# Kernel optimization log

Hardware: AMD Instinct MI355X
Metric: run time of the kernel (lower is better)

## Reference

```python
import jax, jax.numpy as jnp
import numpy as np

VOCAB = 32000
EMB = 256
DEC = 1024
ENC = 1024  # 2 * encoder hidden (bi-directional)
B = 128
S = 512


def setup_inputs() -> dict:
    key = jax.random.key(0)
    ks = jax.random.split(key, 16)
    s = 0.02
    return {
        "inputs": jax.random.randint(ks[0], (B, 1), 0, VOCAB),
        "decoder_hidden": jax.random.normal(ks[1], (B, DEC), jnp.float32),
        "encoder_output": jax.random.normal(ks[2], (B, S, ENC), jnp.float32),
        "emb": jax.random.normal(ks[3], (VOCAB, EMB), jnp.float32) * s,
        "W1": jax.random.normal(ks[4], (ENC, DEC), jnp.float32) * s,
        "b1": jnp.zeros((DEC,), jnp.float32),
        "W2": jax.random.normal(ks[5], (DEC, DEC), jnp.float32) * s,
        "b2": jnp.zeros((DEC,), jnp.float32),
        "Wv": jax.random.normal(ks[6], (DEC, 1), jnp.float32) * s,
        "bv": jnp.zeros((1,), jnp.float32),
        "lstm_k": jax.random.normal(ks[7], (ENC + EMB, 4 * DEC), jnp.float32) * s,
        "lstm_rk": jax.random.normal(ks[8], (DEC, 4 * DEC), jnp.float32) * s,
        "lstm_b": jnp.zeros((4 * DEC,), jnp.float32),
        "fc_W": jax.random.normal(ks[9], (DEC, VOCAB), jnp.float32) * s,
        "fc_b": jnp.zeros((VOCAB,), jnp.float32),
    }


def reference(inputs, decoder_hidden, encoder_output, emb, W1, b1, W2, b2,
              Wv, bv, lstm_k, lstm_rk, lstm_b, fc_W, fc_b):
    # Bahdanau additive attention
    # score: (B, S, 1)
    hidden_proj = decoder_hidden @ W2 + b2                      # (B, DEC)
    score = jnp.tanh(encoder_output @ W1 + b1 + hidden_proj[:, None, :]) @ Wv + bv
    attention_weights = jax.nn.softmax(score, axis=1)           # (B, S, 1)
    context = jnp.sum(attention_weights * encoder_output, axis=1)  # (B, ENC)

    # embedding lookup of the single input token, concat [context, embed]
    x = jnp.concatenate([context, emb[inputs[:, 0]]], axis=-1)  # (B, ENC+EMB)

    # single-step LSTM. Original calls rnn(inputs) with NO initial_state,
    # so h0 = c0 = 0 and the recurrent kernel contributes nothing this step.
    z = x @ lstm_k + lstm_b + jnp.zeros((B, DEC), x.dtype) @ lstm_rk  # (B, 4*DEC)
    i, f, g, o = jnp.split(z, 4, axis=-1)  # keras gate order i,f,c,o
    c = jax.nn.sigmoid(f) * 0.0 + jax.nn.sigmoid(i) * jnp.tanh(g)
    h = jax.nn.sigmoid(o) * jnp.tanh(c)

    logits = h @ fc_W + fc_b                                    # (B, VOCAB)
    return logits, (h, c), attention_weights
```

## Files before the change

### kernel.cpp

```cpp
#include <hip/hip_runtime.h>
#include <hip/hip_bf16.h>
#include <stdint.h>

#define VOCAB 32000
#define EMB   256
#define DEC   1024
#define ENC   1024
#define BB    128
#define SS    512
#define MTOT  (BB * SS)
#define XCOLS (ENC + EMB)
#define NG    (4 * DEC)

typedef _Float16 half8  __attribute__((ext_vector_type(8)));
typedef _Float16 half4  __attribute__((ext_vector_type(4)));
typedef float    floatx4 __attribute__((ext_vector_type(4)));

__device__ __forceinline__ float fast_tanh(float x) {
    float e = __builtin_amdgcn_exp2f(x * 2.885390082f);
    return 1.0f - 2.0f * __builtin_amdgcn_rcpf(e + 1.0f);
}
__device__ __forceinline__ float fast_sigmoid(float x) {
    float e = __builtin_amdgcn_exp2f(-x * 1.442695041f);
    return __builtin_amdgcn_rcpf(1.0f + e);
}

__device__ __forceinline__ void gl_lds16(const void* g, void* l) {
    __builtin_amdgcn_global_load_lds(
        (const __attribute__((address_space(1))) uint32_t*)g,
        (__attribute__((address_space(3))) uint32_t*)l,
        16, 0, 0);
}

__global__ void k_transpose_w1(const float* __restrict__ W1, _Float16* __restrict__ w1t) {
    __shared__ float tile[32][33];
    const int k0 = blockIdx.y * 32, n0 = blockIdx.x * 32;
    const int tx = threadIdx.x, ty = threadIdx.y;
    #pragma unroll
    for (int j = 0; j < 4; ++j)
        tile[ty + j * 8][tx] = W1[(size_t)(k0 + ty + j * 8) * DEC + n0 + tx];
    __syncthreads();
    #pragma unroll
    for (int j = 0; j < 4; ++j)
        w1t[(size_t)(n0 + ty + j * 8) * ENC + k0 + tx] = (_Float16)tile[tx][ty + j * 8];
}

__global__ void k_convert(const float* __restrict__ src, _Float16* __restrict__ dst) {
    const int stride = gridDim.x * blockDim.x;
    const int n8 = (MTOT * ENC) / 8;
    for (int i = blockIdx.x * blockDim.x + threadIdx.x; i < n8; i += stride) {
        floatx4 a = ((const floatx4*)src)[2 * i];
        floatx4 b = ((const floatx4*)src)[2 * i + 1];
        half8 h;
        #pragma unroll
        for (int e = 0; e < 4; ++e) { h[e] = (_Float16)a[e]; h[e + 4] = (_Float16)b[e]; }
        ((half8*)dst)[i] = h;
    }
}

__global__ void k_hidden_proj(const float* __restrict__ dh, const float* __restrict__ W2,
                              const float* __restrict__ b1, const float* __restrict__ b2,
                              float* __restrict__ hp) {
    __shared__ float xs[8 * 1024];
    const int t = threadIdx.x;
    const int n = blockIdx.x * 128 + t;
    const int b0 = blockIdx.y * 8;
    for (int i = t; i < 2048; i += 128)
        ((floatx4*)xs)[i] = ((const floatx4*)(dh + (size_t)b0 * 1024))[i];
    __syncthreads();
    float acc[8] = {0, 0, 0, 0, 0, 0, 0, 0};
    for (int k = 0; k < 1024; ++k) {
        float wval = W2[(size_t)k * 1024 + n];
        #pragma unroll
        for (int j = 0; j < 8; ++j) acc[j] += xs[j * 1024 + k] * wval;
    }
    const float bias = b1[n] + b2[n];
    #pragma unroll
    for (int j = 0; j < 8; ++j) hp[(size_t)(b0 + j) * 1024 + n] = acc[j] + bias;
}

__global__ __launch_bounds__(256) void k_score_f16(
    const _Float16* __restrict__ ench, const _Float16* __restrict__ w1t,
    const float* __restrict__ hp, const float* __restrict__ wv,
    float* __restrict__ scores)
{
    __shared__ _Float16 As[128 * 32];
    __shared__ _Float16 Bs[128 * 32];
    const int g   = blockIdx.x;
    const int xcd = g & 7;
    const int n0  = ((g >> 3) & 7) * 128;
    const int m0  = ((xcd << 6) + (g >> 6)) << 7;
    const int b   = m0 >> 9;
    const int t = threadIdx.x;
    const int lane = t & 63, w = t >> 6;
    const int wm = (w >> 1) * 64, wn = (w & 1) * 64;
    const int col = lane & 15, q = lane >> 4;

    floatx4 acc[4][4];
    #pragma unroll
    for (int i = 0; i < 4; ++i)
        #pragma unroll
        for (int j = 0; j < 4; ++j) acc[i][j] = (floatx4){0.f, 0.f, 0.f, 0.f};

    const int srow = w * 32 + (lane >> 2);
    const int scol = (lane & 3) * 8;
    const _Float16* agp = ench + (size_t)(m0 + srow) * ENC + scol;
    const _Float16* bgp = w1t  + (size_t)(n0 + srow) * ENC + scol;
    _Float16* alp = &As[(w * 32) * 32];
    _Float16* blp = &Bs[(w * 32) * 32];

    for (int k0 = 0; k0 < ENC; k0 += 32) {
        __syncthreads();
        gl_lds16(agp + k0,                alp);
        gl_lds16(agp + k0 + (size_t)16 * ENC, alp + 16 * 32);
        gl_lds16(bgp + k0,                blp);
        gl_lds16(bgp + k0 + (size_t)16 * ENC, blp + 16 * 32);
        __syncthreads();
        half8 af[4], bf[4];
        #pragma unroll
        for (int i = 0; i < 4; ++i)
            af[i] = *(const half8*)(&As[(wm + i * 16 + col) * 32 + q * 8]);
        #pragma unroll
        for (int j = 0; j < 4; ++j)
            bf[j] = *(const half8*)(&Bs[(wn + j * 16 + col) * 32 + q * 8]);
        #pragma unroll
        for (int i = 0; i < 4; ++i)
            #pragma unroll
            for (int j = 0; j < 4; ++j)
                acc[i][j] = __builtin_amdgcn_mfma_f32_16x16x32_f16(af[i], bf[j], acc[i][j], 0, 0, 0);
    }

    float hpv[4], wvv[4];
    #pragma unroll
    for (int j = 0; j < 4; ++j) {
        int n = n0 + wn + j * 16 + col;
        hpv[j] = hp[b * 1024 + n];
        wvv[j] = wv[n];
    }
    #pragma unroll
    for (int i = 0; i < 4; ++i) {
        float rs0 = 0.f, rs1 = 0.f, rs2 = 0.f, rs3 = 0.f;
        #pragma unroll
        for (int j = 0; j < 4; ++j) {
            rs0 += fast_tanh(acc[i][j][0] + hpv[j]) * wvv[j];
            rs1 += fast_tanh(acc[i][j][1] + hpv[j]) * wvv[j];
            rs2 += fast_tanh(acc[i][j][2] + hpv[j]) * wvv[j];
            rs3 += fast_tanh(acc[i][j][3] + hpv[j]) * wvv[j];
        }
        #pragma unroll
        for (int off = 1; off < 16; off <<= 1) {
            rs0 += __shfl_xor(rs0, off);
            rs1 += __shfl_xor(rs1, off);
            rs2 += __shfl_xor(rs2, off);
            rs3 += __shfl_xor(rs3, off);
        }
        if (col == 0) {
            const int mrow = m0 + wm + i * 16 + q * 4;
            atomicAdd(&scores[mrow + 0], rs0);
            atomicAdd(&scores[mrow + 1], rs1);
            atomicAdd(&scores[mrow + 2], rs2);
            atomicAdd(&scores[mrow + 3], rs3);
        }
    }
}

__global__ __launch_bounds__(256) void k_score(
    const float* __restrict__ enc, const _Float16* __restrict__ w1t,
    const float* __restrict__ hp, const float* __restrict__ wv,
    float* __restrict__ scores)
{
    __shared__ _Float16 As[128 * 40];
    __shared__ _Float16 Bs[128 * 40];
    const int n0 = blockIdx.x * 128;
    const int m0 = blockIdx.y * 128;
    const int b  = m0 >> 9;
    const int t = threadIdx.x;
    const int lane = t & 63, w = t >> 6;
    const int wm = (w >> 1) * 64, wn = (w & 1) * 64;
    const int col = lane & 15, q = lane >> 4;

    floatx4 acc[4][4];
    #pragma unroll
    for (int i = 0; i < 4; ++i)
        #pragma unroll
        for (int j = 0; j < 4; ++j) acc[i][j] = (floatx4){0.f, 0.f, 0.f, 0.f};

    const int sr = t >> 1;
    const int sc = (t & 1) * 16;
    const float*    ag = enc + (size_t)(m0 + sr) * ENC + sc;
    const _Float16* bg = w1t + (size_t)(n0 + sr) * ENC + sc;
    _Float16* asw = &As[sr * 40 + sc];
    _Float16* bsw = &Bs[sr * 40 + sc];

    for (int k0 = 0; k0 < ENC; k0 += 32) {
        __syncthreads();
        floatx4 a0 = *(const floatx4*)(ag + k0);
        floatx4 a1 = *(const floatx4*)(ag + k0 + 4);
        floatx4 a2 = *(const floatx4*)(ag + k0 + 8);
        floatx4 a3 = *(const floatx4*)(ag + k0 + 12);
        half8 bv0 = *(const half8*)(bg + k0);
        half8 bv1 = *(const half8*)(bg + k0 + 8);
        half8 ha, hb;
        #pragma unroll
        for (int e = 0; e < 4; ++e) { ha[e] = (_Float16)a0[e]; ha[e + 4] = (_Float16)a1[e]; }
        #pragma unroll
        for (int e = 0; e < 4; ++e) { hb[e] = (_Float16)a2[e]; hb[e + 4] = (_Float16)a3[e]; }
        *(half8*)(asw)     = ha;
        *(half8*)(asw + 8) = hb;
        *(half8*)(bsw)     = bv0;
        *(half8*)(bsw + 8) = bv1;
        __syncthreads();
        half8 af[4], bf[4];
        #pragma unroll
        for (int i = 0; i < 4; ++i)
            af[i] = *(const half8*)(&As[(wm + i * 16 + col) * 40 + q * 8]);
        #pragma unroll
        for (int j = 0; j < 4; ++j)
            bf[j] = *(const half8*)(&Bs[(wn + j * 16 + col) * 40 + q * 8]);
        #pragma unroll
        for (int i = 0; i < 4; ++i)
            #pragma unroll
            for (int j = 0; j < 4; ++j)
                acc[i][j] = __builtin_amdgcn_mfma_f32_16x16x32_f16(af[i], bf[j], acc[i][j], 0, 0, 0);
    }

    float hpv[4], wvv[4];
    #pragma unroll
    for (int j = 0; j < 4; ++j) {
        int n = n0 + wn + j * 16 + col;
        hpv[j] = hp[b * 1024 + n];
        wvv[j] = wv[n];
    }
    #pragma unroll
    for (int i = 0; i < 4; ++i) {
        float rs0 = 0.f, rs1 = 0.f, rs2 = 0.f, rs3 = 0.f;
        #pragma unroll
        for (int j = 0; j < 4; ++j) {
            rs0 += fast_tanh(acc[i][j][0] + hpv[j]) * wvv[j];
            rs1 += fast_tanh(acc[i][j][1] + hpv[j]) * wvv[j];
            rs2 += fast_tanh(acc[i][j][2] + hpv[j]) * wvv[j];
            rs3 += fast_tanh(acc[i][j][3] + hpv[j]) * wvv[j];
        }
        #pragma unroll
        for (int off = 1; off < 16; off <<= 1) {
            rs0 += __shfl_xor(rs0, off);
            rs1 += __shfl_xor(rs1, off);
            rs2 += __shfl_xor(rs2, off);
            rs3 += __shfl_xor(rs3, off);
        }
        if (col == 0) {
            const int mrow = m0 + wm + i * 16 + q * 4;
            atomicAdd(&scores[mrow + 0], rs0);
            atomicAdd(&scores[mrow + 1], rs1);
            atomicAdd(&scores[mrow + 2], rs2);
            atomicAdd(&scores[mrow + 3], rs3);
        }
    }
}

__global__ void k_softmax_emb(const float* __restrict__ scores, const int* __restrict__ tok,
                              const float* __restrict__ emb, float* __restrict__ aw,
                              float* __restrict__ x) {
    const int b = blockIdx.x, t = threadIdx.x;
    float s0 = scores[b * SS + t];
    float s1 = scores[b * SS + 256 + t];
    float mx = fmaxf(s0, s1);
    for (int off = 32; off; off >>= 1) mx = fmaxf(mx, __shfl_xor(mx, off));
    __shared__ float redm[4], reds[4];
    const int w = t >> 6, lane = t & 63;
    if (lane == 0) redm[w] = mx;
    __syncthreads();
    mx = fmaxf(fmaxf(redm[0], redm[1]), fmaxf(redm[2], redm[3]));
    float e0 = exp2f((s0 - mx) * 1.44269504f);
    float e1 = exp2f((s1 - mx) * 1.44269504f);
    float sm = e0 + e1;
    for (int off = 32; off; off >>= 1) sm += __shfl_xor(sm, off);
    if (lane == 0) reds[w] = sm;
    __syncthreads();
    sm = reds[0] + reds[1] + reds[2] + reds[3];
    const float inv = 1.0f / sm;
    aw[b * SS + t]       = e0 * inv;
    aw[b * SS + 256 + t] = e1 * inv;
    x[(size_t)b * XCOLS + ENC + t] = emb[(size_t)tok[b] * EMB + t];
}

__global__ void k_context(const float* __restrict__ enc, const float* __restrict__ aw,
                          float* __restrict__ x) {
    const int b = blockIdx.x >> 2;
    const int e = (blockIdx.x & 3) * 256 + threadIdx.x;
    const float* ep = enc + (size_t)b * SS * ENC + e;
    const float* ap = aw + b * SS;
    float acc = 0.f;
    #pragma unroll 8
    for (int s = 0; s < SS; ++s) acc += ap[s] * ep[(size_t)s * ENC];
    x[(size_t)b * XCOLS + e] = acc;
}

__global__ void k_lstm(const float* __restrict__ x, const float* __restrict__ lk,
                       float* __restrict__ z) {
    __shared__ float xs[8 * XCOLS];
    const int t = threadIdx.x;
    const int n = blockIdx.x * 128 + t;
    const int b0 = blockIdx.y * 8;
    for (int i = t; i < 2560; i += 128)
        ((floatx4*)xs)[i] = ((const floatx4*)(x + (size_t)b0 * XCOLS))[i];
    __syncthreads();
    float acc[8] = {0, 0, 0, 0, 0, 0, 0, 0};
    for (int k = 0; k < XCOLS; ++k) {
        float wval = lk[(size_t)k * NG + n];
        #pragma unroll
        for (int j = 0; j < 8; ++j) acc[j] += xs[j * XCOLS + k] * wval;
    }
    #pragma unroll
    for (int j = 0; j < 8; ++j) z[(size_t)(b0 + j) * NG + n] = acc[j];
}

__global__ void k_gates(const float* __restrict__ z, const float* __restrict__ lb,
                        float* __restrict__ h_out, float* __restrict__ c_out) {
    const int idx = blockIdx.x * 256 + threadIdx.x;
    const int b = idx >> 10, d = idx & 1023;
    const float* zb = z + (size_t)b * NG;
    float iv = zb[d]        + lb[d];
    float gv = zb[d + 2048] + lb[d + 2048];
    float ov = zb[d + 3072] + lb[d + 3072];
    float c = fast_sigmoid(iv) * fast_tanh(gv);
    float h = fast_sigmoid(ov) * fast_tanh(c);
    h_out[idx] = h;
    c_out[idx] = c;
}

__global__ __launch_bounds__(256) void k_fc(
    const float* __restrict__ hsrc, const float* __restrict__ fcW,
    const float* __restrict__ fcb, float* __restrict__ logits)
{
    __shared__ _Float16 As[128 * 40];
    __shared__ _Float16 Bs[128 * 40];
    const int n0 = blockIdx.x * 128;
    const int t = threadIdx.x;
    const int lane = t & 63, w = t >> 6;
    const int wm = (w >> 1) * 64, wn = (w & 1) * 64;
    const int col = lane & 15, q = lane >> 4;

    floatx4 acc[4][4];
    #pragma unroll
    for (int i = 0; i < 4; ++i)
        #pragma unroll
        for (int j = 0; j < 4; ++j) acc[i][j] = (floatx4){0.f, 0.f, 0.f, 0.f};

    const int sr = t >> 1, sc = (t & 1) * 16;
    const float* ag = hsrc + (size_t)sr * 1024 + sc;
    _Float16* asw = &As[sr * 40 + sc];
    const int bn = (t & 31) * 4;
    const int bk = (t >> 5) * 4;

    for (int k0 = 0; k0 < 1024; k0 += 32) {
        __syncthreads();
        floatx4 a0 = *(const floatx4*)(ag + k0);
        floatx4 a1 = *(const floatx4*)(ag + k0 + 4);
        floatx4 a2 = *(const floatx4*)(ag + k0 + 8);
        floatx4 a3 = *(const floatx4*)(ag + k0 + 12);
        half8 ha, hb;
        #pragma unroll
        for (int e = 0; e < 4; ++e) { ha[e] = (_Float16)a0[e]; ha[e + 4] = (_Float16)a1[e]; }
        #pragma unroll
        for (int e = 0; e < 4; ++e) { hb[e] = (_Float16)a2[e]; hb[e + 4] = (_Float16)a3[e]; }
        *(half8*)(asw)     = ha;
        *(half8*)(asw + 8) = hb;
        floatx4 w0 = *(const floatx4*)(fcW + (size_t)(k0 + bk + 0) * VOCAB + n0 + bn);
        floatx4 w1 = *(const floatx4*)(fcW + (size_t)(k0 + bk + 1) * VOCAB + n0 + bn);
        floatx4 w2 = *(const floatx4*)(fcW + (size_t)(k0 + bk + 2) * VOCAB + n0 + bn);
        floatx4 w3 = *(const floatx4*)(fcW + (size_t)(k0 + bk + 3) * VOCAB + n0 + bn);
        #pragma unroll
        for (int c = 0; c < 4; ++c) {
            half4 p = { (_Float16)w0[c], (_Float16)w1[c], (_Float16)w2[c], (_Float16)w3[c] };
            *(half4*)(&Bs[(bn + c) * 40 + bk]) = p;
        }
        __syncthreads();
        half8 af[4], bf[4];
        #pragma unroll
        for (int i = 0; i < 4; ++i)
            af[i] = *(const half8*)(&As[(wm + i * 16 + col) * 40 + q * 8]);
        #pragma unroll
        for (int j = 0; j < 4; ++j)
            bf[j] = *(const half8*)(&Bs[(wn + j * 16 + col) * 40 + q * 8]);
        #pragma unroll
        for (int i = 0; i < 4; ++i)
            #pragma unroll
            for (int j = 0; j < 4; ++j)
                acc[i][j] = __builtin_amdgcn_mfma_f32_16x16x32_f16(af[i], bf[j], acc[i][j], 0, 0, 0);
    }

    float fcbv[4];
    #pragma unroll
    for (int j = 0; j < 4; ++j) fcbv[j] = fcb[n0 + wn + j * 16 + col];
    #pragma unroll
    for (int i = 0; i < 4; ++i)
        #pragma unroll
        for (int j = 0; j < 4; ++j)
            #pragma unroll
            for (int r = 0; r < 4; ++r) {
                const int row = wm + i * 16 + q * 4 + r;
                logits[(size_t)row * VOCAB + n0 + wn + j * 16 + col] = acc[i][j][r] + fcbv[j];
            }
}

extern "C" void kernel_launch(void* const* d_in, const int* in_sizes, int n_in,
                              void* d_out, int out_size, void* d_ws, size_t ws_size,
                              hipStream_t stream) {
    const int*   tok    = (const int*)d_in[0];
    const float* dh     = (const float*)d_in[1];
    const float* enc    = (const float*)d_in[2];
    const float* emb    = (const float*)d_in[3];
    const float* W1     = (const float*)d_in[4];
    const float* b1     = (const float*)d_in[5];
    const float* W2     = (const float*)d_in[6];
    const float* b2     = (const float*)d_in[7];
    const float* Wv     = (const float*)d_in[8];
    const float* lstm_k = (const float*)d_in[10];
    const float* lstm_b = (const float*)d_in[12];
    const float* fc_W   = (const float*)d_in[13];
    const float* fc_b   = (const float*)d_in[14];

    float* out    = (float*)d_out;
    float* logits = out;
    float* h_out  = out + 4096000;
    float* c_out  = out + 4096000 + 131072;
    float* aw     = out + 4096000 + 262144;

    char* ws = (char*)d_ws;
    _Float16* w1t    = (_Float16*)ws;
    float*    hp     = (float*)(ws + 2097152);
    float*    scores = (float*)(ws + 2621440);
    float*    x      = (float*)(ws + 2883584);
    float*    z      = (float*)(ws + 3538944);
    _Float16* ench   = (_Float16*)(ws + 6291456);

    const size_t need_fast = 6291456 + (size_t)MTOT * ENC * sizeof(_Float16);
    const bool fast = ws_size >= need_fast;

    hipMemsetAsync(scores, 0, MTOT * sizeof(float), stream);
    k_transpose_w1<<<dim3(32, 32), dim3(32, 8), 0, stream>>>(W1, w1t);
    k_hidden_proj<<<dim3(8, 16), 128, 0, stream>>>(dh, W2, b1, b2, hp);
    if (fast) {
        k_convert<<<2048, 256, 0, stream>>>(enc, ench);
        k_score_f16<<<4096, 256, 0, stream>>>(ench, w1t, hp, Wv, scores);
    } else {
        k_score<<<dim3(8, 512), 256, 0, stream>>>(enc, w1t, hp, Wv, scores);
    }
    k_softmax_emb<<<128, 256, 0, stream>>>(scores, tok, emb, aw, x);
    k_context<<<512, 256, 0, stream>>>(enc, aw, x);
    k_lstm<<<dim3(32, 16), 128, 0, stream>>>(x, lstm_k, z);
    k_gates<<<512, 256, 0, stream>>>(z, lstm_b, h_out, c_out);
    k_fc<<<250, 256, 0, stream>>>(h_out, fc_W, fc_b, logits);
}
```

Measured before the change: 975.5 us.

## Fuse prep kernels, split-K small GEMMs, drop score atomics, read fp16 encoder for context

Combines the fp32-to-fp16 encoder conversion, the W1 transpose and a split-K hidden projection into one launch. Score partials are written per N-block through an LDS reduction instead of global atomics, which also removes the memset on the fast path. The context reduction now reads the fp16 encoder copy and is split over two sequence halves, and the LSTM GEMM uses split-K with the embedding gather fused in. Workspace regions are reused aggressively (z2 overlays w1t, ctx2 overlays scores8), and the fp16 context adds rounding error.

```diff
diff --git a/kernel.cpp b/kernel.cpp
--- a/kernel.cpp
+++ b/kernel.cpp
@@ -11,6 +11,7 @@
 #define MTOT  (BB * SS)
 #define XCOLS (ENC + EMB)
 #define NG    (4 * DEC)
+#define BD    (BB * DEC)
 
 typedef _Float16 half8  __attribute__((ext_vector_type(8)));
 typedef _Float16 half4  __attribute__((ext_vector_type(4)));
@@ -32,65 +33,79 @@
         16, 0, 0);
 }
 
-__global__ void k_transpose_w1(const float* __restrict__ W1, _Float16* __restrict__ w1t) {
+__global__ __launch_bounds__(256) void k_prep(
+    const float* __restrict__ enc, _Float16* __restrict__ ench,
+    const float* __restrict__ W1, _Float16* __restrict__ w1t,
+    const float* __restrict__ dh, const float* __restrict__ W2,
+    const float* __restrict__ b1, const float* __restrict__ b2,
+    float* __restrict__ hp4, int do_convert)
+{
     __shared__ float tile[32][33];
-    const int k0 = blockIdx.y * 32, n0 = blockIdx.x * 32;
-    const int tx = threadIdx.x, ty = threadIdx.y;
-    #pragma unroll
-    for (int j = 0; j < 4; ++j)
-        tile[ty + j * 8][tx] = W1[(size_t)(k0 + ty + j * 8) * DEC + n0 + tx];
-    __syncthreads();
-    #pragma unroll
-    for (int j = 0; j < 4; ++j)
-        w1t[(size_t)(n0 + ty + j * 8) * ENC + k0 + tx] = (_Float16)tile[tx][ty + j * 8];
-}
-
-__global__ void k_convert(const float* __restrict__ src, _Float16* __restrict__ dst) {
-    const int stride = gridDim.x * blockDim.x;
-    const int n8 = (MTOT * ENC) / 8;
-    for (int i = blockIdx.x * blockDim.x + threadIdx.x; i < n8; i += stride) {
-        floatx4 a = ((const floatx4*)src)[2 * i];
-        floatx4 b = ((const floatx4*)src)[2 * i + 1];
-        half8 h;
-        #pragma unroll
-        for (int e = 0; e < 4; ++e) { h[e] = (_Float16)a[e]; h[e + 4] = (_Float16)b[e]; }
-        ((half8*)dst)[i] = h;
-    }
-}
-
-__global__ void k_hidden_proj(const float* __restrict__ dh, const float* __restrict__ W2,
-                              const float* __restrict__ b1, const float* __restrict__ b2,
-                              float* __restrict__ hp) {
-    __shared__ float xs[8 * 1024];
-    const int t = threadIdx.x;
-    const int n = blockIdx.x * 128 + t;
-    const int b0 = blockIdx.y * 8;
-    for (int i = t; i < 2048; i += 128)
-        ((floatx4*)xs)[i] = ((const floatx4*)(dh + (size_t)b0 * 1024))[i];
-    __syncthreads();
-    float acc[8] = {0, 0, 0, 0, 0, 0, 0, 0};
-    for (int k = 0; k < 1024; ++k) {
-        float wval = W2[(size_t)k * 1024 + n];
-        #pragma unroll
-        for (int j = 0; j < 8; ++j) acc[j] += xs[j * 1024 + k] * wval;
-    }
-    const float bias = b1[n] + b2[n];
-    #pragma unroll
-    for (int j = 0; j < 8; ++j) hp[(size_t)(b0 + j) * 1024 + n] = acc[j] + bias;
+    __shared__ float xs[8 * 256];
+    const int bid = blockIdx.x, t = threadIdx.x;
+
+    if (bid < 2048) {
+        if (!do_convert) return;
+        const int base = bid * 4096 + t;
+        #pragma unroll
+        for (int it = 0; it < 16; ++it) {
+            const int i = base + it * 256;
+            floatx4 a = ((const floatx4*)enc)[2 * i];
+            floatx4 c = ((const floatx4*)enc)[2 * i + 1];
+            half8 h;
+            #pragma unroll
+            for (int e = 0; e < 4; ++e) { h[e] = (_Float16)a[e]; h[e + 4] = (_Float16)c[e]; }
+            ((half8*)ench)[i] = h;
+        }
+    } else if (bid < 3072) {
+        const int p = bid - 2048;
+        const int n0 = (p & 31) * 32, k0 = (p >> 5) * 32;
+        const int tx = t & 31, ty = t >> 5;
+        #pragma unroll
+        for (int j = 0; j < 4; ++j)
+            tile[ty + j * 8][tx] = W1[(size_t)(k0 + ty + j * 8) * DEC + n0 + tx];
+        __syncthreads();
+        #pragma unroll
+        for (int j = 0; j < 4; ++j)
+            w1t[(size_t)(n0 + ty + j * 8) * ENC + k0 + tx] = (_Float16)tile[tx][ty + j * 8];
+    } else {
+        const int p  = bid - 3072;
+        const int n  = (p & 3) * 256 + t;
+        const int b0 = ((p >> 2) & 15) * 8;
+        const int kz = p >> 6;
+        const int k0 = kz * 256;
+        for (int i = t; i < 2048; i += 256) {
+            const int j = i >> 8, kk = i & 255;
+            xs[i] = dh[(size_t)(b0 + j) * 1024 + k0 + kk];
+        }
+        __syncthreads();
+        float acc[8] = {0, 0, 0, 0, 0, 0, 0, 0};
+        for (int k = 0; k < 256; ++k) {
+            const float wval = W2[(size_t)(k0 + k) * 1024 + n];
+            #pragma unroll
+            for (int j = 0; j < 8; ++j) acc[j] += xs[j * 256 + k] * wval;
+        }
+        const float bias = (kz == 0) ? (b1[n] + b2[n]) : 0.0f;
+        #pragma unroll
+        for (int j = 0; j < 8; ++j)
+            hp4[(size_t)kz * BD + (size_t)(b0 + j) * 1024 + n] = acc[j] + bias;
+    }
 }
 
 __global__ __launch_bounds__(256) void k_score_f16(
     const _Float16* __restrict__ ench, const _Float16* __restrict__ w1t,
-    const float* __restrict__ hp, const float* __restrict__ wv,
-    float* __restrict__ scores)
+    const float* __restrict__ hp4, const float* __restrict__ wv,
+    float* __restrict__ scores8)
 {
     __shared__ _Float16 As[128 * 32];
     __shared__ _Float16 Bs[128 * 32];
-    const int g   = blockIdx.x;
-    const int xcd = g & 7;
-    const int n0  = ((g >> 3) & 7) * 128;
-    const int m0  = ((xcd << 6) + (g >> 6)) << 7;
-    const int b   = m0 >> 9;
+    __shared__ float red[2][128];
+    const int g    = blockIdx.x;
+    const int xcd  = g & 7;
+    const int nblk = (g >> 3) & 7;
+    const int n0   = nblk * 128;
+    const int m0   = ((xcd << 6) + (g >> 6)) << 7;
+    const int b    = m0 >> 9;
     const int t = threadIdx.x;
     const int lane = t & 63, w = t >> 6;
     const int wm = (w >> 1) * 64, wn = (w & 1) * 64;
@@ -111,9 +126,9 @@
 
     for (int k0 = 0; k0 < ENC; k0 += 32) {
         __syncthreads();
-        gl_lds16(agp + k0,                alp);
+        gl_lds16(agp + k0,                    alp);
         gl_lds16(agp + k0 + (size_t)16 * ENC, alp + 16 * 32);
-        gl_lds16(bgp + k0,                blp);
+        gl_lds16(bgp + k0,                    blp);
         gl_lds16(bgp + k0 + (size_t)16 * ENC, blp + 16 * 32);
         __syncthreads();
         half8 af[4], bf[4];
@@ -133,8 +148,9 @@
     float hpv[4], wvv[4];
     #pragma unroll
     for (int j = 0; j < 4; ++j) {
-        int n = n0 + wn + j * 16 + col;
-        hpv[j] = hp[b * 1024 + n];
+        const int n = n0 + wn + j * 16 + col;
+        const size_t base = (size_t)b * 1024 + n;
+        hpv[j] = hp4[base] + hp4[BD + base] + hp4[2 * BD + base] + hp4[3 * BD + base];
         wvv[j] = wv[n];
     }
     #pragma unroll
@@ -155,19 +171,22 @@
             rs3 += __shfl_xor(rs3, off);
         }
         if (col == 0) {
-            const int mrow = m0 + wm + i * 16 + q * 4;
-            atomicAdd(&scores[mrow + 0], rs0);
-            atomicAdd(&scores[mrow + 1], rs1);
-            atomicAdd(&scores[mrow + 2], rs2);
-            atomicAdd(&scores[mrow + 3], rs3);
-        }
-    }
+            const int r = wm + i * 16 + q * 4;
+            red[w & 1][r + 0] = rs0;
+            red[w & 1][r + 1] = rs1;
+            red[w & 1][r + 2] = rs2;
+            red[w & 1][r + 3] = rs3;
+        }
+    }
+    __syncthreads();
+    if (t < 128)
+        scores8[(size_t)nblk * MTOT + m0 + t] = red[0][t] + red[1][t];
 }
 
 __global__ __launch_bounds__(256) void k_score(
     const float* __restrict__ enc, const _Float16* __restrict__ w1t,
-    const float* __restrict__ hp, const float* __restrict__ wv,
-    float* __restrict__ scores)
+    const float* __restrict__ hp4, const float* __restrict__ wv,
+    float* __restrict__ scores8)
 {
     __shared__ _Float16 As[128 * 40];
     __shared__ _Float16 Bs[128 * 40];
@@ -227,8 +246,9 @@
     float hpv[4], wvv[4];
     #pragma unroll
     for (int j = 0; j < 4; ++j) {
-        int n = n0 + wn + j * 16 + col;
-        hpv[j] = hp[b * 1024 + n];
+        const int n = n0 + wn + j * 16 + col;
+        const size_t base = (size_t)b * 1024 + n;
+        hpv[j] = hp4[base] + hp4[BD + base] + hp4[2 * BD + base] + hp4[3 * BD + base];
         wvv[j] = wv[n];
     }
     #pragma unroll
@@ -250,20 +270,22 @@
         }
         if (col == 0) {
             const int mrow = m0 + wm + i * 16 + q * 4;
-            atomicAdd(&scores[mrow + 0], rs0);
-            atomicAdd(&scores[mrow + 1], rs1);
-            atomicAdd(&scores[mrow + 2], rs2);
-            atomicAdd(&scores[mrow + 3], rs3);
-        }
-    }
-}
-
-__global__ void k_softmax_emb(const float* __restrict__ scores, const int* __restrict__ tok,
-                              const float* __restrict__ emb, float* __restrict__ aw,
-                              float* __restrict__ x) {
+            atomicAdd(&scores8[mrow + 0], rs0);
+            atomicAdd(&scores8[mrow + 1], rs1);
+            atomicAdd(&scores8[mrow + 2], rs2);
+            atomicAdd(&scores8[mrow + 3], rs3);
+        }
+    }
+}
+
+__global__ void k_softmax(const float* __restrict__ scores8, float* __restrict__ aw) {
     const int b = blockIdx.x, t = threadIdx.x;
-    float s0 = scores[b * SS + t];
-    float s1 = scores[b * SS + 256 + t];
+    float s0 = 0.f, s1 = 0.f;
+    #pragma unroll
+    for (int nb = 0; nb < 8; ++nb) {
+        s0 += scores8[(size_t)nb * MTOT + b * SS + t];
+        s1 += scores8[(size_t)nb * MTOT + b * SS + 256 + t];
+    }
     float mx = fmaxf(s0, s1);
     for (int off = 32; off; off >>= 1) mx = fmaxf(mx, __shfl_xor(mx, off));
     __shared__ float redm[4], reds[4];
@@ -281,48 +303,92 @@
     const float inv = 1.0f / sm;
     aw[b * SS + t]       = e0 * inv;
     aw[b * SS + 256 + t] = e1 * inv;
-    x[(size_t)b * XCOLS + ENC + t] = emb[(size_t)tok[b] * EMB + t];
-}
-
-__global__ void k_context(const float* __restrict__ enc, const float* __restrict__ aw,
-                          float* __restrict__ x) {
-    const int b = blockIdx.x >> 2;
-    const int e = (blockIdx.x & 3) * 256 + threadIdx.x;
-    const float* ep = enc + (size_t)b * SS * ENC + e;
-    const float* ap = aw + b * SS;
-    float acc = 0.f;
+}
+
+__global__ void k_context_f16(const _Float16* __restrict__ ench, const float* __restrict__ aw,
+                              float* __restrict__ ctx2) {
+    const int b  = blockIdx.x >> 1;
+    const int sz = blockIdx.x & 1;
+    const int s0 = sz * 256;
+    const int e4 = threadIdx.x;
+    const _Float16* ep = ench + ((size_t)b * SS + s0) * ENC + e4 * 4;
+    const float* ap = aw + b * SS + s0;
+    float a0 = 0.f, a1 = 0.f, a2 = 0.f, a3 = 0.f;
     #pragma unroll 8
-    for (int s = 0; s < SS; ++s) acc += ap[s] * ep[(size_t)s * ENC];
-    x[(size_t)b * XCOLS + e] = acc;
-}
-
-__global__ void k_lstm(const float* __restrict__ x, const float* __restrict__ lk,
-                       float* __restrict__ z) {
-    __shared__ float xs[8 * XCOLS];
+    for (int s = 0; s < 256; ++s) {
+        const float a = ap[s];
+        half4 v = *(const half4*)(ep + (size_t)s * ENC);
+        a0 += a * (float)v[0]; a1 += a * (float)v[1];
+        a2 += a * (float)v[2]; a3 += a * (float)v[3];
+    }
+    floatx4 r = {a0, a1, a2, a3};
+    *(floatx4*)(ctx2 + (size_t)sz * BD + (size_t)b * 1024 + e4 * 4) = r;
+}
+
+__global__ void k_context_f32(const float* __restrict__ enc, const float* __restrict__ aw,
+                              float* __restrict__ ctx2) {
+    const int b  = blockIdx.x >> 1;
+    const int sz = blockIdx.x & 1;
+    const int s0 = sz * 256;
+    const int e4 = threadIdx.x;
+    const float* ep = enc + ((size_t)b * SS + s0) * ENC + e4 * 4;
+    const float* ap = aw + b * SS + s0;
+    float a0 = 0.f, a1 = 0.f, a2 = 0.f, a3 = 0.f;
+    #pragma unroll 4
+    for (int s = 0; s < 256; ++s) {
+        const float a = ap[s];
+        floatx4 v = *(const floatx4*)(ep + (size_t)s * ENC);
+        a0 += a * v[0]; a1 += a * v[1]; a2 += a * v[2]; a3 += a * v[3];
+    }
+    floatx4 r = {a0, a1, a2, a3};
+    *(floatx4*)(ctx2 + (size_t)sz * BD + (size_t)b * 1024 + e4 * 4) = r;
+}
+
+__global__ void k_lstm(const float* __restrict__ ctx2, const float* __restrict__ emb,
+                       const int* __restrict__ tok, const float* __restrict__ lk,
+                       float* __restrict__ z2) {
+    __shared__ float xs[8 * 640];
     const int t = threadIdx.x;
-    const int n = blockIdx.x * 128 + t;
+    const int n = blockIdx.x * 256 + t;
     const int b0 = blockIdx.y * 8;
-    for (int i = t; i < 2560; i += 128)
-        ((floatx4*)xs)[i] = ((const floatx4*)(x + (size_t)b0 * XCOLS))[i];
+    const int kz = blockIdx.z;
+    const int k0 = kz * 640;
+    #pragma unroll
+    for (int j = 0; j < 8; ++j) {
+        const int bb = b0 + j;
+        const int tk = tok[bb];
+        for (int kk = t; kk < 640; kk += 256) {
+            const int gk = k0 + kk;
+            float v;
+            if (gk < 1024)
+                v = ctx2[(size_t)bb * 1024 + gk] + ctx2[(size_t)BD + (size_t)bb * 1024 + gk];
+            else
+                v = emb[(size_t)tk * EMB + gk - 1024];
+            xs[j * 640 + kk] = v;
+        }
+    }
     __syncthreads();
     float acc[8] = {0, 0, 0, 0, 0, 0, 0, 0};
-    for (int k = 0; k < XCOLS; ++k) {
-        float wval = lk[(size_t)k * NG + n];
-        #pragma unroll
-        for (int j = 0; j < 8; ++j) acc[j] += xs[j * XCOLS + k] * wval;
-    }
-    #pragma unroll
-    for (int j = 0; j < 8; ++j) z[(size_t)(b0 + j) * NG + n] = acc[j];
-}
-
-__global__ void k_gates(const float* __restrict__ z, const float* __restrict__ lb,
+    #pragma unroll 4
+    for (int k = 0; k < 640; ++k) {
+        const float wval = lk[(size_t)(k0 + k) * NG + n];
+        #pragma unroll
+        for (int j = 0; j < 8; ++j) acc[j] += xs[j * 640 + k] * wval;
+    }
+    #pragma unroll
+    for (int j = 0; j < 8; ++j)
+        z2[(size_t)kz * BB * NG + (size_t)(b0 + j) * NG + n] = acc[j];
+}
+
+__global__ void k_gates(const float* __restrict__ z2, const float* __restrict__ lb,
                         float* __restrict__ h_out, float* __restrict__ c_out) {
     const int idx = blockIdx.x * 256 + threadIdx.x;
     const int b = idx >> 10, d = idx & 1023;
-    const float* zb = z + (size_t)b * NG;
-    float iv = zb[d]        + lb[d];
-    float gv = zb[d + 2048] + lb[d + 2048];
-    float ov = zb[d + 3072] + lb[d + 3072];
+    const float* z0 = z2 + (size_t)b * NG;
+    const float* z1 = z2 + (size_t)BB * NG + (size_t)b * NG;
+    float iv = z0[d]        + z1[d]        + lb[d];
+    float gv = z0[d + 2048] + z1[d + 2048] + lb[d + 2048];
+    float ov = z0[d + 3072] + z1[d + 3072] + lb[d + 3072];
     float c = fast_sigmoid(iv) * fast_tanh(gv);
     float h = fast_sigmoid(ov) * fast_tanh(c);
     h_out[idx] = h;
@@ -428,28 +494,29 @@
     float* aw     = out + 4096000 + 262144;
 
     char* ws = (char*)d_ws;
-    _Float16* w1t    = (_Float16*)ws;
-    float*    hp     = (float*)(ws + 2097152);
-    float*    scores = (float*)(ws + 2621440);
-    float*    x      = (float*)(ws + 2883584);
-    float*    z      = (float*)(ws + 3538944);
-    _Float16* ench   = (_Float16*)(ws + 6291456);
-
-    const size_t need_fast = 6291456 + (size_t)MTOT * ENC * sizeof(_Float16);
+    _Float16* w1t     = (_Float16*)ws;
+    float*    hp4     = (float*)(ws + (2u << 20));
+    float*    scores8 = (float*)(ws + (4u << 20));
+    float*    ctx2    = (float*)(ws + (4u << 20));
+    float*    z2      = (float*)ws;
+    _Float16* ench    = (_Float16*)(ws + (6u << 20));
+
+    const size_t need_fast = (6u << 20) + (size_t)MTOT * ENC * sizeof(_Float16);
     const bool fast = ws_size >= need_fast;
 
-    hipMemsetAsync(scores, 0, MTOT * sizeof(float), stream);
-    k_transpose_w1<<<dim3(32, 32), dim3(32, 8), 0, stream>>>(W1, w1t);
-    k_hidden_proj<<<dim3(8, 16), 128, 0, stream>>>(dh, W2, b1, b2, hp);
     if (fast) {
-        k_convert<<<2048, 256, 0, stream>>>(enc, ench);
-        k_score_f16<<<4096, 256, 0, stream>>>(ench, w1t, hp, Wv, scores);
+        k_prep<<<3328, 256, 0, stream>>>(enc, ench, W1, w1t, dh, W2, b1, b2, hp4, 1);
+        k_score_f16<<<4096, 256, 0, stream>>>(ench, w1t, hp4, Wv, scores8);
+        k_softmax<<<128, 256, 0, stream>>>(scores8, aw);
+        k_context_f16<<<256, 256, 0, stream>>>(ench, aw, ctx2);
     } else {
-        k_score<<<dim3(8, 512), 256, 0, stream>>>(enc, w1t, hp, Wv, scores);
-    }
-    k_softmax_emb<<<128, 256, 0, stream>>>(scores, tok, emb, aw, x);
-    k_context<<<512, 256, 0, stream>>>(enc, aw, x);
-    k_lstm<<<dim3(32, 16), 128, 0, stream>>>(x, lstm_k, z);
-    k_gates<<<512, 256, 0, stream>>>(z, lstm_b, h_out, c_out);
+        k_prep<<<3328, 256, 0, stream>>>(enc, ench, W1, w1t, dh, W2, b1, b2, hp4, 0);
+        hipMemsetAsync(scores8, 0, 8 * MTOT * sizeof(float), stream);
+        k_score<<<dim3(8, 512), 256, 0, stream>>>(enc, w1t, hp4, Wv, scores8);
+        k_softmax<<<128, 256, 0, stream>>>(scores8, aw);
+        k_context_f32<<<256, 256, 0, stream>>>(enc, aw, ctx2);
+    }
+    k_lstm<<<dim3(16, 16, 2), 256, 0, stream>>>(ctx2, emb, tok, lstm_k, z2);
+    k_gates<<<512, 256, 0, stream>>>(z2, lstm_b, h_out, c_out);
     k_fc<<<250, 256, 0, stream>>>(h_out, fc_W, fc_b, logits);
 }
```

Result: faster. 848.5 us (-13.0%).
